# Optimization experiments

Hardware: AMD Instinct MI355X
Metric: run time of the kernel (lower is better)

The kernel has to match this reference:

```python
import jax, jax.numpy as jnp
import numpy as np

N = 20000          # nodes
E = 640000         # edges
IN_F, CL1_F, CL2_F, OUT_F = 128, 256, 128, 10
K = 4              # Chebyshev order
EPS = 1e-5         # BatchNorm eps
LAMBDA_MAX = 2.0   # PyG ChebConv default


def setup_inputs() -> dict:
    key = jax.random.key(0)
    ks = jax.random.split(key, 8)
    x = jax.random.normal(ks[0], (N, IN_F), dtype=jnp.float32)
    edge_index = jax.random.randint(ks[1], (2, E), 0, N, dtype=jnp.int64)
    edge_weight = jax.random.uniform(ks[2], (E,), dtype=jnp.float32)
    W1 = jax.random.normal(ks[3], (K, IN_F, CL1_F), dtype=jnp.float32) * 0.05
    b1 = jnp.zeros((CL1_F,), jnp.float32)
    W2 = jax.random.normal(ks[4], (K, CL1_F, CL2_F), dtype=jnp.float32) * 0.05
    b2 = jnp.zeros((CL2_F,), jnp.float32)
    gamma1 = jnp.ones((CL1_F,), jnp.float32); beta1 = jnp.zeros((CL1_F,), jnp.float32)
    gamma2 = jnp.ones((CL2_F,), jnp.float32); beta2 = jnp.zeros((CL2_F,), jnp.float32)
    Wlin = jax.random.normal(ks[5], (OUT_F, CL2_F), dtype=jnp.float32) * 0.05
    blin = jnp.zeros((OUT_F,), jnp.float32)
    return {"x": x, "edge_index": edge_index, "edge_weight": edge_weight,
            "W1": W1, "b1": b1, "W2": W2, "b2": b2,
            "gamma1": gamma1, "beta1": beta1, "gamma2": gamma2, "beta2": beta2,
            "Wlin": Wlin, "blin": blin}


def _cheb_norm(edge_index, edge_weight, n):
    # Scaled Laplacian L_hat = (2/lambda_max) * (I - D^{-1/2} A D^{-1/2}) - I
    # (matches PyG ChebConv __norm__ with normalization='sym').
    row, col = edge_index[0], edge_index[1]
    w = jnp.where(row == col, 0.0, edge_weight)  # remove_self_loops
    deg = jax.ops.segment_sum(w, row, num_segments=n)
    dis = jnp.where(deg > 0, 1.0 / jnp.sqrt(deg), 0.0)
    w_norm = -(dis[row] * w * dis[col]) * (2.0 / LAMBDA_MAX)
    diag_w = 2.0 / LAMBDA_MAX - 1.0  # = 0 for lambda_max=2
    return row, col, w_norm, diag_w


def _cheb_conv(x, row, col, w_norm, diag_w, W, b):
    n = x.shape[0]

    def spmm(t):  # L_hat @ t : gather sources, scale, scatter-add to targets
        return jax.ops.segment_sum(w_norm[:, None] * t[row], col, num_segments=n) + diag_w * t

    Tx0 = x
    out = Tx0 @ W[0]
    Tx1 = spmm(Tx0)
    out = out + Tx1 @ W[1]
    for k in range(2, W.shape[0]):  # Chebyshev recursion T_k = 2 L_hat T_{k-1} - T_{k-2}
        Tx2 = 2.0 * spmm(Tx1) - Tx0
        out = out + Tx2 @ W[k]
        Tx0, Tx1 = Tx1, Tx2
    return out + b


def _batchnorm(x, gamma, beta):  # training-mode BN over the node axis
    m = x.mean(axis=0)
    v = x.var(axis=0)
    return gamma * (x - m) / jnp.sqrt(v + EPS) + beta


def reference(x, edge_index, edge_weight, W1, b1, W2, b2,
              gamma1, beta1, gamma2, beta2, Wlin, blin):
    row, col, w_norm, diag_w = _cheb_norm(edge_index, edge_weight, x.shape[0])
    h = jax.nn.relu(_cheb_conv(x, row, col, w_norm, diag_w, W1, b1))
    h = _batchnorm(h, gamma1, beta1)
    h = jax.nn.relu(_cheb_conv(h, row, col, w_norm, diag_w, W2, b2))
    h = _batchnorm(h, gamma2, beta2)
    return h @ Wlin.T + blin  # [N, OUT_F]
```

## Files before the change

### kernel.cpp

```cpp
#include <hip/hip_runtime.h>
#include <cstdint>
#include <cstddef>

#define NNODES 20000
#define NEDGES 640000
#define IN_F   128
#define CL1_F  256
#define CL2_F  128
#define OUT_F  10
#define BN_EPS 1e-5f

#define NC     256
#define CE     (NEDGES / NC)
#define HALFN  10000

#define CONVN  (512 * 256 + 4 * 256 * 128 + NNODES * 128)

typedef unsigned short u16;


__device__ __forceinline__ float bf2f(u16 u) {
    union { uint32_t i; float f; } v; v.i = ((uint32_t)u) << 16; return v.f;
}
__device__ __forceinline__ u16 f2bf(float f) {
    union { float f; uint32_t i; } v; v.f = f;
    uint32_t r = v.i + 0x7fffu + ((v.i >> 16) & 1u);
    return (u16)(r >> 16);
}
__device__ __forceinline__ void bf2x2(uint32_t u, float& lo, float& hi) {
    union { uint32_t i; float f; } a, b;
    a.i = u << 16; b.i = u & 0xffff0000u;
    lo = a.f; hi = b.f;
}
__device__ __forceinline__ uint32_t f2bf2(float lo, float hi) {
    return (uint32_t)f2bf(lo) | ((uint32_t)f2bf(hi) << 16);
}
__device__ __forceinline__ void unpack8(uint4 v, float* o) {
    bf2x2(v.x, o[0], o[1]); bf2x2(v.y, o[2], o[3]);
    bf2x2(v.z, o[4], o[5]); bf2x2(v.w, o[6], o[7]);
}


__launch_bounds__(256)
__global__ void build_hist_conv(const int* __restrict__ ei, const float* __restrict__ ew,
                                u16* __restrict__ cnt_h, u16* __restrict__ degq_h,
                                const float* __restrict__ W1, u16* __restrict__ W1t,
                                const float* __restrict__ W2, u16* __restrict__ W2t,
                                const float* __restrict__ x, u16* __restrict__ A1,
                                int E, int N) {
    __shared__ uint32_t scnt[HALFN / 2];
    __shared__ uint32_t sdeg[HALFN / 2];
    int b = blockIdx.x;
    if (b < NC) {
        int e0 = b * CE, e1 = e0 + CE;
        for (int half = 0; half < 2; ++half) {
            int lo = half * HALFN;
            for (int i = threadIdx.x; i < HALFN / 2; i += 256) { scnt[i] = 0; sdeg[i] = 0; }
            __syncthreads();
            for (int e = e0 + threadIdx.x; e < e1; e += 256) {
                int r = ei[e];
                int c = ei[E + e];
                int ci = c - lo;
                if ((unsigned)ci < HALFN) atomicAdd(&scnt[ci >> 1], 1u << ((ci & 1) * 16));
                int ri = r - lo;
                if ((unsigned)ri < HALFN) {
                    float w = (r == c) ? 0.0f : ew[e];
                    uint32_t q = (uint32_t)(w * 1024.0f + 0.5f);
                    atomicAdd(&sdeg[ri >> 1], q << ((ri & 1) * 16));
                }
            }
            __syncthreads();
            for (int i = threadIdx.x; i < HALFN; i += 256) {
                cnt_h[(size_t)b * N + lo + i]  = (u16)((scnt[i >> 1] >> ((i & 1) * 16)) & 0xffffu);
                degq_h[(size_t)b * N + lo + i] = (u16)((sdeg[i >> 1] >> ((i & 1) * 16)) & 0xffffu);
            }
            __syncthreads();
        }
    } else {
        int i = (b - NC) * 256 + threadIdx.x;
        const int S1 = 512 * 256;
        const int S2 = 4 * 256 * 128;
        const int SX = NNODES * 128;
        if (i < S1) {
            int k = i / 256, n = i - k * 256;
            W1t[(size_t)n * 512 + k] = f2bf(W1[i]);
        } else if (i < S1 + S2) {
            int j = i - S1;
            int kc = j / (256 * 128);
            int rem = j - kc * 256 * 128;
            int ci = rem / 128, co = rem - ci * 128;
            W2t[(size_t)(kc * 128 + co) * 256 + ci] = f2bf(W2[j]);
        } else if (i < S1 + S2 + SX) {
            int j = i - S1 - S2;
            int n = j >> 7, f = j & 127;
            A1[(size_t)n * 512 + f] = f2bf(x[j]);
        }
    }
}

__global__ void reduce_dis_base(const u16* __restrict__ cnt_h, const u16* __restrict__ degq_h,
                                int* __restrict__ tot, float* __restrict__ dis,
                                u16* __restrict__ baseD, int N) {
    int i = blockIdx.x * blockDim.x + threadIdx.x;
    if (i >= N) return;
    int t = 0;
    uint32_t dq = 0;
#pragma unroll 8
    for (int c = 0; c < NC; ++c) {
        baseD[(size_t)c * N + i] = (u16)t;
        t  += cnt_h[(size_t)c * N + i];
        dq += degq_h[(size_t)c * N + i];
    }
    tot[i] = t;
    float d = (float)dq * (1.0f / 1024.0f);
    dis[i] = (d > 0.0f) ? rsqrtf(d) : 0.0f;
}

__global__ void scan_kernel(const int* __restrict__ tot, int* __restrict__ rowptr, int N) {
    __shared__ int sums[256];
    int t = threadIdx.x;
    int per = (N + 255) / 256;
    int s0 = t * per, s1 = min(s0 + per, N);
    int s = 0;
    for (int i = s0; i < s1; ++i) s += tot[i];
    sums[t] = s;
    __syncthreads();
    if (t == 0) {
        int run = 0;
        for (int i = 0; i < 256; ++i) { int v = sums[i]; sums[i] = run; run += v; }
        rowptr[N] = run;
    }
    __syncthreads();
    int run = sums[t];
    for (int i = s0; i < s1; ++i) { rowptr[i] = run; run += tot[i]; }
}

__launch_bounds__(256)
__global__ void fill_kernel(const int* __restrict__ ei, const float* __restrict__ ew,
                            const float* __restrict__ dis, const int* __restrict__ rowptr,
                            const u16* __restrict__ baseD,
                            uint32_t* __restrict__ erec, int E, int N) {
    __shared__ uint32_t srank[NNODES / 2];
    int chunk = blockIdx.x;
    int e0 = chunk * CE, e1 = e0 + CE;
    for (int i = threadIdx.x; i < NNODES / 2; i += 256) srank[i] = 0;
    __syncthreads();
    for (int e = e0 + threadIdx.x; e < e1; e += 256) {
        int r = ei[e];
        int c = ei[E + e];
        float w = (r == c) ? 0.0f : ew[e];
        float wn = -(dis[r] * w * dis[c]);
        int sh = (c & 1) * 16;
        uint32_t old = atomicAdd(&srank[c >> 1], 1u << sh);
        int rank = (old >> sh) & 0xffff;
        int pos = rowptr[c] + (int)baseD[(size_t)chunk * N + c] + rank;
        erec[pos] = (uint32_t)r | ((uint32_t)f2bf(wn) << 16);
    }
}

__launch_bounds__(256)
__global__ void spmm_cl(const int* __restrict__ rowptr, const uint32_t* __restrict__ erec,
                        const u16* __restrict__ tin, int ldi,
                        const u16* __restrict__ t1, int ld1, float c1,
                        const u16* __restrict__ t2, int ld2, float c2,
                        u16* __restrict__ tout, int ldo,
                        const float* __restrict__ bias, int doReluBias,
                        int N, float s) {
    int gid = blockIdx.x * blockDim.x + threadIdx.x;
    int n = gid >> 4;
    if (n >= N) return;
    int f = (gid & 15) << 3;
    int p = rowptr[n], pe = rowptr[n + 1];
    float acc[8] = {};
    for (; p + 7 < pe; p += 8) {
        uint32_t rr[8];
#pragma unroll
        for (int u = 0; u < 8; ++u) rr[u] = erec[p + u];
        uint4 vv[8];
#pragma unroll
        for (int u = 0; u < 8; ++u)
            vv[u] = *(const uint4*)(tin + (size_t)(rr[u] & 0xffffu) * ldi + f);
#pragma unroll
        for (int u = 0; u < 8; ++u) {
            float w = bf2f((u16)(rr[u] >> 16));
            float fa[8];
            unpack8(vv[u], fa);
#pragma unroll
            for (int q = 0; q < 8; ++q) acc[q] += w * fa[q];
        }
    }
    for (; p < pe; ++p) {
        uint32_t r0 = erec[p];
        uint4 v0 = *(const uint4*)(tin + (size_t)(r0 & 0xffffu) * ldi + f);
        float w0 = bf2f((u16)(r0 >> 16));
        float fa[8];
        unpack8(v0, fa);
#pragma unroll
        for (int q = 0; q < 8; ++q) acc[q] += w0 * fa[q];
    }
#pragma unroll
    for (int q = 0; q < 8; ++q) acc[q] *= s;
    if (t1) {
        uint4 v = *(const uint4*)(t1 + (size_t)n * ld1 + f);
        float fv[8]; unpack8(v, fv);
#pragma unroll
        for (int q = 0; q < 8; ++q) acc[q] += c1 * fv[q];
    }
    if (t2) {
        uint4 v = *(const uint4*)(t2 + (size_t)n * ld2 + f);
        float fv[8]; unpack8(v, fv);
#pragma unroll
        for (int q = 0; q < 8; ++q) acc[q] += c2 * fv[q];
    }
    if (doReluBias) {
#pragma unroll
        for (int q = 0; q < 8; ++q) acc[q] = fmaxf(acc[q] + bias[f + q], 0.0f);
    }
    uint4 o;
    o.x = f2bf2(acc[0], acc[1]);
    o.y = f2bf2(acc[2], acc[3]);
    o.z = f2bf2(acc[4], acc[5]);
    o.w = f2bf2(acc[6], acc[7]);
    *(uint4*)(tout + (size_t)n * ldo + f) = o;
}


typedef __attribute__((ext_vector_type(8))) short short8;
typedef __attribute__((ext_vector_type(4))) float floatx4;

#define GBM 64
#define GBN 64
#define GBK 64

__launch_bounds__(256)
__global__ void gemm_mfma(const u16* __restrict__ A, const u16* __restrict__ Bt,
                          const float* __restrict__ bias, void* __restrict__ Cout,
                          float* __restrict__ ssum, float* __restrict__ ssq,
                          int M, int N, int K, int doRelu, int outBf) {
    __shared__ __align__(16) u16 As[GBM][GBK + 8];
    __shared__ __align__(16) u16 Bs[GBN][GBK + 8];
    __shared__ float colsum[GBN], colsq[GBN];

    int tid = threadIdx.x;
    int lane = tid & 63;
    int wave = tid >> 6;
    int wm = (wave & 1) * 32;
    int wn = (wave >> 1) * 32;
    int rowBase = blockIdx.x * GBM;
    int colBase = blockIdx.y * GBN;

    floatx4 acc[2][2];
#pragma unroll
    for (int i = 0; i < 2; ++i)
#pragma unroll
        for (int j = 0; j < 2; ++j) {
            acc[i][j][0] = 0.f; acc[i][j][1] = 0.f; acc[i][j][2] = 0.f; acc[i][j][3] = 0.f;
        }

    int sr = tid >> 3;
    int sc = (tid & 7) * 8;

    for (int k0 = 0; k0 < K; k0 += GBK) {
#pragma unroll
        for (int h = 0; h < 2; ++h) {
            int r = sr + h * 32;
            int gm = rowBase + r;
            uint4 v = make_uint4(0, 0, 0, 0);
            if (gm < M) v = *(const uint4*)(A + (size_t)gm * K + k0 + sc);
            *(uint4*)&As[r][sc] = v;
            int gn = colBase + r;
            uint4 w = *(const uint4*)(Bt + (size_t)gn * K + k0 + sc);
            *(uint4*)&Bs[r][sc] = w;
        }
        __syncthreads();

        int mrow = lane & 15;
        int kq = (lane >> 4) * 8;
#pragma unroll
        for (int kk = 0; kk < GBK; kk += 32) {
            short8 af[2], bfr[2];
#pragma unroll
            for (int i = 0; i < 2; ++i) af[i] = *(const short8*)&As[wm + i * 16 + mrow][kk + kq];
#pragma unroll
            for (int j = 0; j < 2; ++j) bfr[j] = *(const short8*)&Bs[wn + j * 16 + mrow][kk + kq];
#pragma unroll
            for (int i = 0; i < 2; ++i)
#pragma unroll
                for (int j = 0; j < 2; ++j)
                    acc[i][j] = __builtin_amdgcn_mfma_f32_16x16x32_bf16(af[i], bfr[j], acc[i][j], 0, 0, 0);
        }
        __syncthreads();
    }

    if (ssum) {
        if (tid < GBN) { colsum[tid] = 0.f; colsq[tid] = 0.f; }
        __syncthreads();
    }

    int cn0 = colBase + wn + (lane & 15);
    int rq = (lane >> 4) * 4;
    float* Cf = (float*)Cout;
    u16*   Cb = (u16*)Cout;
#pragma unroll
    for (int j = 0; j < 2; ++j) {
        float ps = 0.f, pq = 0.f;
        int n = cn0 + j * 16;
#pragma unroll
        for (int i = 0; i < 2; ++i) {
#pragma unroll
            for (int r = 0; r < 4; ++r) {
                int m = rowBase + wm + i * 16 + rq + r;
                if (m >= M) continue;
                float v = acc[i][j][r];
                if (bias) v += bias[n];
                if (doRelu) v = fmaxf(v, 0.0f);
                if (outBf) {
                    u16 bb = f2bf(v);
                    Cb[(size_t)m * N + n] = bb;
                    if (ssum) { float vb = bf2f(bb); ps += vb; pq += vb * vb; }
                } else {
                    Cf[(size_t)m * N + n] = v;
                }
            }
        }
        if (ssum) {
            int lc = wn + j * 16 + (lane & 15);
            atomicAdd(&colsum[lc], ps);
            atomicAdd(&colsq[lc], pq);
        }
    }
    if (ssum) {
        __syncthreads();
        if (tid < GBN) {
            atomicAdd(&ssum[colBase + tid], colsum[tid]);
            atomicAdd(&ssq[colBase + tid], colsq[tid]);
        }
    }
}


#define BN_ROWS 64
__global__ void bn_stats_bf(const u16* __restrict__ h, int N, int C,
                            float* __restrict__ sums, float* __restrict__ sumsq) {
    int c = threadIdx.x;
    int r0 = blockIdx.x * BN_ROWS;
    int r1 = min(r0 + BN_ROWS, N);
    float s = 0.f, q = 0.f;
    for (int r = r0; r < r1; ++r) {
        float v = bf2f(h[(size_t)r * C + c]);
        s += v;
        q += v * v;
    }
    atomicAdd(&sums[c], s);
    atomicAdd(&sumsq[c], q);
}

__launch_bounds__(256)
__global__ void fold_w2(u16* __restrict__ W2t, const float* __restrict__ sums,
                        const float* __restrict__ sumsq, const float* __restrict__ gamma,
                        const float* __restrict__ beta, float* __restrict__ rowvec, float invN) {
    __shared__ float red[4];
    int n = blockIdx.x;
    int k = threadIdx.x;
    float m = sums[k] * invN;
    float var = sumsq[k] * invN - m * m;
    float sc = gamma[k] / sqrtf(var + BN_EPS);
    float sh = beta[k] - m * sc;
    float wf = bf2f(W2t[(size_t)n * 256 + k]);
    W2t[(size_t)n * 256 + k] = f2bf(wf * sc);
    float part = sh * wf;
#pragma unroll
    for (int off = 32; off > 0; off >>= 1) part += __shfl_down(part, off);
    if ((k & 63) == 0) red[k >> 6] = part;
    __syncthreads();
    if (k == 0) rowvec[n] = red[0] + red[1] + red[2] + red[3];
}


__global__ void final_linear_bn(const u16* __restrict__ g, const float* __restrict__ Wlin,
                                const float* __restrict__ blin, const float* __restrict__ sums,
                                const float* __restrict__ sumsq, const float* __restrict__ gamma,
                                const float* __restrict__ beta, float* __restrict__ out,
                                int N, float invN) {
    __shared__ float Ws[OUT_F * CL2_F];
    __shared__ float bs[OUT_F];
    __shared__ float scs[CL2_F], shs[CL2_F];
    for (int i = threadIdx.x; i < OUT_F * CL2_F; i += 256) Ws[i] = Wlin[i];
    if (threadIdx.x < OUT_F) bs[threadIdx.x] = blin[threadIdx.x];
    if (threadIdx.x < CL2_F) {
        int c = threadIdx.x;
        float m = sums[c] * invN;
        float var = sumsq[c] * invN - m * m;
        float sc = gamma[c] / sqrtf(var + BN_EPS);
        scs[c] = sc;
        shs[c] = beta[c] - m * sc;
    }
    __syncthreads();
    int idx = blockIdx.x * 256 + threadIdx.x;
    if (idx >= N * OUT_F) return;
    int n = idx / OUT_F, o = idx - n * OUT_F;
    const u16* gr = g + (size_t)n * CL2_F;
    const float* wr = Ws + o * CL2_F;
    float acc = 0.f;
#pragma unroll 8
    for (int f = 0; f < CL2_F; ++f) acc += (bf2f(gr[f]) * scs[f] + shs[f]) * wr[f];
    out[idx] = acc + bs[o];
}


extern "C" void kernel_launch(void* const* d_in, const int* in_sizes, int n_in,
                              void* d_out, int out_size, void* d_ws, size_t ws_size,
                              hipStream_t stream) {
    const float* x      = (const float*)d_in[0];
    const int*   ei     = (const int*)d_in[1];
    const float* ew     = (const float*)d_in[2];
    const float* W1     = (const float*)d_in[3];
    const float* b1     = (const float*)d_in[4];
    const float* W2     = (const float*)d_in[5];
    const float* b2     = (const float*)d_in[6];
    const float* gamma1 = (const float*)d_in[7];
    const float* beta1  = (const float*)d_in[8];
    const float* gamma2 = (const float*)d_in[9];
    const float* beta2  = (const float*)d_in[10];
    const float* Wlin   = (const float*)d_in[11];
    const float* blin   = (const float*)d_in[12];
    float* out = (float*)d_out;

    const int N = NNODES, E = NEDGES;

    char* base = (char*)d_ws;
    u16*     cnt_h  = (u16*)    (base + 0);
    u16*     degq_h = (u16*)    (base + 10240000);
    u16*     baseD  = (u16*)    (base + 20480000);
    u16*     A1     = (u16*)    (base + 30720000);
    u16*     Hc     = A1;
    u16*     h1bf   = (u16*)    (base + 51200000);
    u16*     pbuf   = (u16*)    (base + 61440000);
    u16*     bb2    = (u16*)    (base + 66560000);
    u16*     bb1    = (u16*)    (base + 71680000);
    uint32_t* erec  = (uint32_t*)(base + 76800000);
    u16*     W1t    = (u16*)    (base + 79360000);
    u16*     W2t    = (u16*)    (base + 79622144);
    float*   rowvec = (float*)  (base + 79884288);
    int*     rowptr = (int*)    (base + 79886336);
    int*     tot    = (int*)    (base + 79966352);
    float*   dis    = (float*)  (base + 80046352);
    float*   bns1   = (float*)  (base + 80126352);
    float*   bnq1    = bns1 + 256;
    float*   bns2    = bnq1 + 256;
    float*   bnq2    = bns2 + 256;

    dim3 blk(256);

    hipMemsetAsync(bns1, 0, 4 * 256 * sizeof(float), stream);

    build_hist_conv<<<dim3(NC + (CONVN + 255) / 256), blk, 0, stream>>>(
        ei, ew, cnt_h, degq_h, W1, W1t, W2, W2t, x, A1, E, N);
    reduce_dis_base<<<dim3((N + 255) / 256), blk, 0, stream>>>(cnt_h, degq_h, tot, dis, baseD, N);
    scan_kernel<<<dim3(1), blk, 0, stream>>>(tot, rowptr, N);
    fill_kernel<<<dim3(NC), blk, 0, stream>>>(ei, ew, dis, rowptr, baseD, erec, E, N);

    dim3 gS(((N << 4) + 255) / 256);

    spmm_cl<<<gS, blk, 0, stream>>>(rowptr, erec, A1 + 0,   512, nullptr,  512, 0.f,
                                    nullptr, 512, 0.f, A1 + 128, 512, nullptr, 0, N, 1.0f);
    spmm_cl<<<gS, blk, 0, stream>>>(rowptr, erec, A1 + 128, 512, A1 + 0,   512, -1.f,
                                    nullptr, 512, 0.f, A1 + 256, 512, nullptr, 0, N, 2.0f);
    spmm_cl<<<gS, blk, 0, stream>>>(rowptr, erec, A1 + 256, 512, A1 + 128, 512, -1.f,
                                    nullptr, 512, 0.f, A1 + 384, 512, nullptr, 0, N, 2.0f);

    gemm_mfma<<<dim3((N + GBM - 1) / GBM, CL1_F / GBN), blk, 0, stream>>>(
        A1, W1t, b1, h1bf, bns1, bnq1, N, CL1_F, 512, 1, 1);

    fold_w2<<<dim3(512), dim3(256), 0, stream>>>(W2t, bns1, bnq1, gamma1, beta1, rowvec, 1.0f / N);

    gemm_mfma<<<dim3((N + GBM - 1) / GBM, 512 / GBN), blk, 0, stream>>>(
        h1bf, W2t, rowvec, Hc, nullptr, nullptr, N, 512, 256, 0, 1);

    spmm_cl<<<gS, blk, 0, stream>>>(rowptr, erec, Hc + 384, 512, Hc + 256, 512, 1.f,
                                    nullptr, 512, 0.f, bb2, 128, nullptr, 0, N, 2.0f);
    spmm_cl<<<gS, blk, 0, stream>>>(rowptr, erec, bb2, 128, Hc + 384, 512, -1.f,
                                    Hc + 128, 512, 1.f, bb1, 128, nullptr, 0, N, 2.0f);
    spmm_cl<<<gS, blk, 0, stream>>>(rowptr, erec, bb1, 128, bb2, 128, -1.f,
                                    Hc + 0, 512, 1.f, pbuf, 128, b2, 1, N, 1.0f);

    bn_stats_bf<<<dim3((N + BN_ROWS - 1) / BN_ROWS), dim3(CL2_F), 0, stream>>>(pbuf, N, CL2_F, bns2, bnq2);

    final_linear_bn<<<dim3((N * OUT_F + 255) / 256), blk, 0, stream>>>(
        pbuf, Wlin, blin, bns2, bnq2, gamma2, beta2, out, N, 1.0f / N);
}
```

Baseline: 379.7 us.

## Vectorize input conversion, parallelize rowptr scan, fold BN into final linear

The x-to-bf16 conversion now has each thread handle 8 features using float4 loads and one uint4 store, which cuts the block count for that part of the setup kernel. The single-block scan now stages tot in padded shared memory, uses a wavefront shuffle prefix sum, and writes rowptr with int4 stores, replacing the serial thread-0 pass over 256 partial sums. The final linear layer folds the BatchNorm scale into the weights and the shift into a per-output constant, then reads its bf16 inputs as 16-byte vectors. Together these target several small serial or uncoalesced costs; the scan assumes N is divisible by 4 and by the chunk size.

Result: faster. 349.6 us (-7.9%).

```diff
diff --git a/kernel.cpp b/kernel.cpp
--- a/kernel.cpp
+++ b/kernel.cpp
@@ -14,7 +14,9 @@
 #define CE     (NEDGES / NC)
 #define HALFN  10000
 
-#define CONVN  (512 * 256 + 4 * 256 * 128 + NNODES * 128)
+#define WB1    512
+#define WB2    512
+#define XB     ((NNODES * 16) / 256)
 
 typedef unsigned short u16;
 
@@ -77,23 +79,26 @@
             __syncthreads();
         }
     } else {
-        int i = (b - NC) * 256 + threadIdx.x;
-        const int S1 = 512 * 256;
-        const int S2 = 4 * 256 * 128;
-        const int SX = NNODES * 128;
-        if (i < S1) {
-            int k = i / 256, n = i - k * 256;
+        int b2 = b - NC;
+        if (b2 < WB1) {
+            int i = b2 * 256 + threadIdx.x;
+            int k = i >> 8, n = i & 255;
             W1t[(size_t)n * 512 + k] = f2bf(W1[i]);
-        } else if (i < S1 + S2) {
-            int j = i - S1;
+        } else if (b2 < WB1 + WB2) {
+            int j = (b2 - WB1) * 256 + threadIdx.x;
             int kc = j / (256 * 128);
             int rem = j - kc * 256 * 128;
-            int ci = rem / 128, co = rem - ci * 128;
+            int ci = rem >> 7, co = rem & 127;
             W2t[(size_t)(kc * 128 + co) * 256 + ci] = f2bf(W2[j]);
-        } else if (i < S1 + S2 + SX) {
-            int j = i - S1 - S2;
-            int n = j >> 7, f = j & 127;
-            A1[(size_t)n * 512 + f] = f2bf(x[j]);
+        } else {
+            int j = (b2 - WB1 - WB2) * 256 + threadIdx.x;
+            int n = j >> 4, f = (j & 15) << 3;
+            const float4* xp = (const float4*)(x + (size_t)n * 128 + f);
+            float4 v0 = xp[0], v1 = xp[1];
+            uint4 o;
+            o.x = f2bf2(v0.x, v0.y); o.y = f2bf2(v0.z, v0.w);
+            o.z = f2bf2(v1.x, v1.y); o.w = f2bf2(v1.z, v1.w);
+            *(uint4*)(A1 + (size_t)n * 512 + f) = o;
         }
     }
 }
@@ -116,23 +121,61 @@
     dis[i] = (d > 0.0f) ? rsqrtf(d) : 0.0f;
 }
 
+
+#define SCHUNK  80
+#define SSTRIDE 81
+
+__launch_bounds__(256)
 __global__ void scan_kernel(const int* __restrict__ tot, int* __restrict__ rowptr, int N) {
-    __shared__ int sums[256];
-    int t = threadIdx.x;
-    int per = (N + 255) / 256;
-    int s0 = t * per, s1 = min(s0 + per, N);
-    int s = 0;
-    for (int i = s0; i < s1; ++i) s += tot[i];
-    sums[t] = s;
-    __syncthreads();
-    if (t == 0) {
-        int run = 0;
-        for (int i = 0; i < 256; ++i) { int v = sums[i]; sums[i] = run; run += v; }
-        rowptr[N] = run;
-    }
-    __syncthreads();
-    int run = sums[t];
-    for (int i = s0; i < s1; ++i) { rowptr[i] = run; run += tot[i]; }
+    __shared__ int s[250 * SSTRIDE];
+    __shared__ int wtot[4];
+    int tid = threadIdx.x;
+
+    const int4* t4 = (const int4*)tot;
+    for (int i4 = tid; i4 < N / 4; i4 += 256) {
+        int4 v = t4[i4];
+        int i = i4 * 4;
+        int c = i / SCHUNK;
+        int idx = c * SSTRIDE + (i - c * SCHUNK);
+        s[idx] = v.x; s[idx + 1] = v.y; s[idx + 2] = v.z; s[idx + 3] = v.w;
+    }
+    __syncthreads();
+
+    int tsum = 0;
+    if (tid < 250) {
+        int base = tid * SSTRIDE;
+#pragma unroll 8
+        for (int j = 0; j < SCHUNK; ++j) tsum += s[base + j];
+    }
+
+    int lane = tid & 63, wv = tid >> 6;
+    int pre = tsum;
+#pragma unroll
+    for (int off = 1; off < 64; off <<= 1) {
+        int v = __shfl_up(pre, off);
+        if (lane >= off) pre += v;
+    }
+    if (lane == 63) wtot[wv] = pre;
+    __syncthreads();
+    int run = pre - tsum;
+    for (int w = 0; w < wv; ++w) run += wtot[w];
+    if (tid == 0) rowptr[N] = wtot[0] + wtot[1] + wtot[2] + wtot[3];
+
+    if (tid < 250) {
+        int base = tid * SSTRIDE;
+        for (int j = 0; j < SCHUNK; ++j) { int v = s[base + j]; s[base + j] = run; run += v; }
+    }
+    __syncthreads();
+
+    int4* r4 = (int4*)rowptr;
+    for (int i4 = tid; i4 < N / 4; i4 += 256) {
+        int i = i4 * 4;
+        int c = i / SCHUNK;
+        int idx = c * SSTRIDE + (i - c * SCHUNK);
+        int4 v;
+        v.x = s[idx]; v.y = s[idx + 1]; v.z = s[idx + 2]; v.w = s[idx + 3];
+        r4[i4] = v;
+    }
 }
 
 __launch_bounds__(256)
@@ -377,34 +420,52 @@
 }
 
 
+__launch_bounds__(256)
 __global__ void final_linear_bn(const u16* __restrict__ g, const float* __restrict__ Wlin,
                                 const float* __restrict__ blin, const float* __restrict__ sums,
                                 const float* __restrict__ sumsq, const float* __restrict__ gamma,
                                 const float* __restrict__ beta, float* __restrict__ out,
                                 int N, float invN) {
-    __shared__ float Ws[OUT_F * CL2_F];
-    __shared__ float bs[OUT_F];
+    __shared__ float Ws2[OUT_F][CL2_F + 4];
     __shared__ float scs[CL2_F], shs[CL2_F];
-    for (int i = threadIdx.x; i < OUT_F * CL2_F; i += 256) Ws[i] = Wlin[i];
-    if (threadIdx.x < OUT_F) bs[threadIdx.x] = blin[threadIdx.x];
-    if (threadIdx.x < CL2_F) {
-        int c = threadIdx.x;
-        float m = sums[c] * invN;
-        float var = sumsq[c] * invN - m * m;
-        float sc = gamma[c] / sqrtf(var + BN_EPS);
-        scs[c] = sc;
-        shs[c] = beta[c] - m * sc;
-    }
-    __syncthreads();
-    int idx = blockIdx.x * 256 + threadIdx.x;
+    __shared__ float oc[OUT_F];
+    int tid = threadIdx.x;
+    if (tid < CL2_F) {
+        float m = sums[tid] * invN;
+        float var = sumsq[tid] * invN - m * m;
+        float sc = gamma[tid] / sqrtf(var + BN_EPS);
+        scs[tid] = sc;
+        shs[tid] = beta[tid] - m * sc;
+    }
+    __syncthreads();
+    for (int i = tid; i < OUT_F * CL2_F; i += 256) {
+        int f = i & 127;
+        Ws2[i >> 7][f] = Wlin[i] * scs[f];
+    }
+    __syncthreads();
+    if (tid < OUT_F) {
+        float a = blin[tid];
+        const float* wr = Wlin + tid * CL2_F;
+        for (int f = 0; f < CL2_F; ++f) a += shs[f] * wr[f];
+        oc[tid] = a;
+    }
+    __syncthreads();
+    int idx = blockIdx.x * 256 + tid;
     if (idx >= N * OUT_F) return;
     int n = idx / OUT_F, o = idx - n * OUT_F;
     const u16* gr = g + (size_t)n * CL2_F;
-    const float* wr = Ws + o * CL2_F;
+    const float* w2 = Ws2[o];
     float acc = 0.f;
-#pragma unroll 8
-    for (int f = 0; f < CL2_F; ++f) acc += (bf2f(gr[f]) * scs[f] + shs[f]) * wr[f];
-    out[idx] = acc + bs[o];
+#pragma unroll
+    for (int f0 = 0; f0 < CL2_F; f0 += 8) {
+        uint4 v = *(const uint4*)(gr + f0);
+        float fa[8]; unpack8(v, fa);
+        const float4* wp = (const float4*)(w2 + f0);
+        float4 wa = wp[0], wb = wp[1];
+        acc += fa[0] * wa.x + fa[1] * wa.y + fa[2] * wa.z + fa[3] * wa.w
+             + fa[4] * wb.x + fa[5] * wb.y + fa[6] * wb.z + fa[7] * wb.w;
+    }
+    out[idx] = acc + oc[o];
 }
 
 
@@ -454,7 +515,7 @@
 
     hipMemsetAsync(bns1, 0, 4 * 256 * sizeof(float), stream);
 
-    build_hist_conv<<<dim3(NC + (CONVN + 255) / 256), blk, 0, stream>>>(
+    build_hist_conv<<<dim3(NC + WB1 + WB2 + XB), blk, 0, stream>>>(
         ei, ew, cnt_h, degq_h, W1, W1t, W2, W2t, x, A1, E, N);
     reduce_dis_base<<<dim3((N + 255) / 256), blk, 0, stream>>>(cnt_h, degq_h, tot, dis, baseD, N);
     scan_kernel<<<dim3(1), blk, 0, stream>>>(tot, rowptr, N);
```
